# Optimization experiments

Hardware: AMD Instinct MI355X
Metric: run time of the kernel (lower is better)

## Reference

```python
import jax, jax.numpy as jnp
import numpy as np

HS = 128  # hidden_size
B, L = 2, 1024


def setup_inputs() -> dict:
    key = jax.random.key(0)
    k = jax.random.split(key, 3)
    d = HS
    X = jax.random.normal(k[0], (B, L, d), dtype=jnp.float32)
    # mlp: Linear(4d -> d), GELU, Linear(d -> 1)
    W1 = jax.random.normal(k[1], (4 * d, d), dtype=jnp.float32) / np.sqrt(4 * d).astype(np.float32)
    b1 = jnp.zeros((d,), dtype=jnp.float32)
    W2 = jax.random.normal(k[2], (d, 1), dtype=jnp.float32) / np.sqrt(d).astype(np.float32)
    b2 = jnp.zeros((1,), dtype=jnp.float32)
    return {"X": X, "W1": W1, "b1": b1, "W2": W2, "b2": b2}


def reference(X, W1, b1, W2, b2):
    # f = cat([Xi, Xj, Xi-Xj, Xi*Xj]) @ W1  decomposes exactly into four matmuls:
    #   Xi@(Wi+Wd) + Xj@(Wj-Wd) + (Xi*Xj)@Wp
    # avoiding the (b,l,l,4d) concat tensor.
    b, l, d = X.shape
    Wi, Wj, Wd, Wp = jnp.split(W1, 4, axis=0)  # each (d, h)
    A = X @ (Wi + Wd)                           # (b,l,h): depends on i only
    Bm = X @ (Wj - Wd)                          # (b,l,h): depends on j only
    P = jnp.einsum('bid,bjd,dh->bijh', X, X, Wp)  # elementwise-product term
    h = jax.nn.gelu(A[:, :, None, :] + Bm[:, None, :, :] + P + b1,
                    approximate=False)          # (b,l,l,h), exact GELU like nn.GELU()
    out = jnp.einsum('bijh,ho->bij', h, W2) + b2[0]  # (b,l,l)
    out = jax.nn.relu(out)
    out = 0.5 * (out + jnp.swapaxes(out, 1, 2))      # symmetrize
    diag_mask = 1.0 - jnp.eye(l, dtype=out.dtype)    # zero the diagonal
    return out * diag_mask
```

## Files before the change

### kernel.cpp

```cpp
#include <hip/hip_runtime.h>


typedef __attribute__((ext_vector_type(8))) short short8;
typedef __attribute__((ext_vector_type(16))) float f32x16;
typedef __attribute__((ext_vector_type(2))) float f32x2;

#define NT 32
#define NTRI 528
#define IPB 8

__device__ __forceinline__ unsigned short f2bf(float f) {
  unsigned int u = __float_as_uint(f);
  u = (u + 0x7fffu + ((u >> 16) & 1u)) >> 16;
  return (unsigned short)u;
}

__device__ __forceinline__ short8 pack8(float4 a, float4 b) {
  short8 r;
  r[0] = (short)f2bf(a.x); r[1] = (short)f2bf(a.y);
  r[2] = (short)f2bf(a.z); r[3] = (short)f2bf(a.w);
  r[4] = (short)f2bf(b.x); r[5] = (short)f2bf(b.y);
  r[6] = (short)f2bf(b.z); r[7] = (short)f2bf(b.w);
  return r;
}

__device__ __forceinline__ f32x2 gelu_2(f32x2 x) {
  f32x2 r = __builtin_elementwise_max(x, (f32x2)0.0f);
  f32x2 w = __builtin_elementwise_fma(r, (f32x2)2.0f, -x);
  f32x2 g = __builtin_elementwise_fma(w, (f32x2)0.00242f, (f32x2)-0.03569f);
  g = __builtin_elementwise_fma(w, g, (f32x2)-0.48287f);
  g = __builtin_elementwise_fma(w, g, (f32x2)-1.13986f);
  g = __builtin_elementwise_fma(w, g, (f32x2)-1.0f);
  f32x2 f;
  f[0] = __builtin_amdgcn_exp2f(g[0]);
  f[1] = __builtin_amdgcn_exp2f(g[1]);
  return __builtin_elementwise_fma(-f, w, r);
}

__global__ void k0_prep_w(const float* __restrict__ W1, unsigned short* __restrict__ wsT) {
  int idx = blockIdx.x * 256 + threadIdx.x;
  int arr = idx >> 14, rem = idx & 16383, h = rem >> 7, d = rem & 127;
  float v;
  if (arr == 0)      v = W1[d * 128 + h] + W1[(256 + d) * 128 + h];
  else if (arr == 1) v = W1[(128 + d) * 128 + h] - W1[(256 + d) * 128 + h];
  else               v = W1[(384 + d) * 128 + h];
  wsT[idx] = f2bf(v);
}

__global__ __launch_bounds__(256) void k1_ab(const float* __restrict__ X,
                                             const unsigned short* __restrict__ wsT,
                                             const float* __restrict__ b1,
                                             float* __restrict__ Aout,
                                             float* __restrict__ Bout) {
  int tid = threadIdx.x, w = tid >> 6, lane = tid & 63, jl = lane & 31, hi = lane >> 5;
  int row0 = blockIdx.x * 64;
  int c0 = w * 64;
  f32x16 a00 = (f32x16)0.f, a01 = (f32x16)0.f, a10 = (f32x16)0.f, a11 = (f32x16)0.f;
#pragma unroll
  for (int s = 0; s < 8; ++s) {
    const float* xp0 = X + (size_t)(row0 + jl) * 128 + s * 16 + hi * 8;
    const float* xp1 = xp0 + 32 * 128;
    short8 fa0 = pack8(*(const float4*)xp0, *(const float4*)(xp0 + 4));
    short8 fa1 = pack8(*(const float4*)xp1, *(const float4*)(xp1 + 4));
    short8 fb0 = *(const short8*)(wsT + (size_t)(c0 + jl) * 128 + s * 16 + hi * 8);
    short8 fb1 = *(const short8*)(wsT + (size_t)(c0 + 32 + jl) * 128 + s * 16 + hi * 8);
    a00 = __builtin_amdgcn_mfma_f32_32x32x16_bf16(fa0, fb0, a00, 0, 0, 0);
    a01 = __builtin_amdgcn_mfma_f32_32x32x16_bf16(fa0, fb1, a01, 0, 0, 0);
    a10 = __builtin_amdgcn_mfma_f32_32x32x16_bf16(fa1, fb0, a10, 0, 0, 0);
    a11 = __builtin_amdgcn_mfma_f32_32x32x16_bf16(fa1, fb1, a11, 0, 0, 0);
  }
  bool isB = (c0 >= 128);
  float b1v0 = 0.f, b1v1 = 0.f;
  if (isB) { b1v0 = b1[c0 - 128 + jl]; b1v1 = b1[c0 - 96 + jl]; }
#pragma unroll
  for (int q = 0; q < 16; ++q) {
    int r = (q & 3) + 8 * (q >> 2) + 4 * hi;
    int bl0 = row0 + r, bl1 = row0 + 32 + r;
    if (!isB) {
      Aout[(size_t)bl0 * 128 + c0 + jl]      = a00[q];
      Aout[(size_t)bl0 * 128 + c0 + 32 + jl] = a01[q];
      Aout[(size_t)bl1 * 128 + c0 + jl]      = a10[q];
      Aout[(size_t)bl1 * 128 + c0 + 32 + jl] = a11[q];
    } else {
      Bout[(size_t)bl0 * 128 + c0 - 128 + jl] = a00[q] + b1v0;
      Bout[(size_t)bl0 * 128 + c0 - 96 + jl]  = a01[q] + b1v1;
      Bout[(size_t)bl1 * 128 + c0 - 128 + jl] = a10[q] + b1v0;
      Bout[(size_t)bl1 * 128 + c0 - 96 + jl]  = a11[q] + b1v1;
    }
  }
}

union BfPack { __bf16 h[16]; short8 v[2]; };

__global__ __launch_bounds__(256) void k2_main(const float* __restrict__ X,
                                               const unsigned short* __restrict__ WpT,
                                               const float* __restrict__ Aws,
                                               const float* __restrict__ Bws,
                                               const float* __restrict__ W2,
                                               const float* __restrict__ b2,
                                               float* __restrict__ out) {
  __shared__ __align__(16) unsigned short Mlds[2][32 * 128];
  __shared__ __align__(16) float Xp[IPB][128];
  __shared__ __align__(16) float Abias[IPB][128];
  __shared__ __align__(16) float Bbias[IPB][128];
  __shared__ __align__(16) float W2l[128];
  __shared__ float2 osum[IPB][4][32];
  __shared__ float valbuf[IPB][33];

  int bid = blockIdx.x;
  int q4 = bid & 3;
  int tl = bid >> 2;
  int b = tl / NTRI;
  int t = tl - b * NTRI;
  int ti = 0;
  while (t >= NT - ti) { t -= NT - ti; ++ti; }
  int tj = ti + t;
  int gi0 = ti * 32, gj0 = tj * 32;
  int giBase = gi0 + q4 * IPB;

  int tid = threadIdx.x, w = tid >> 6, lane = tid & 63, jl = lane & 31, hi = lane >> 5;
  int dseg = tid >> 5;
  int gj = gj0 + jl;
  const size_t rowX = (size_t)b * 1024;

  {
    int r = tid >> 5, c = (tid & 31) * 4;
    const float* xp = X   + (rowX + giBase + r) * 128 + c;
    const float* ap = Aws + (rowX + giBase + r) * 128 + c;
    const float* bp = Bws + (rowX + giBase + r) * 128 + c;
    *(float4*)(&Xp[r][c])    = *(const float4*)(xp);
    *(float4*)(&Abias[r][c]) = *(const float4*)(ap);
    *(float4*)(&Bbias[r][c]) = *(const float4*)(bp);
    if (tid < 128) W2l[tid] = W2[tid];
  }

  float xj[16], bmj[16], ajv[16];
  {
    const float* xjp = X + (rowX + gj) * 128 + dseg * 16;
    *(float4*)(xj + 0)  = *(const float4*)(xjp + 0);
    *(float4*)(xj + 4)  = *(const float4*)(xjp + 4);
    *(float4*)(xj + 8)  = *(const float4*)(xjp + 8);
    *(float4*)(xj + 12) = *(const float4*)(xjp + 12);
  }
#pragma unroll
  for (int g = 0; g < 4; ++g) {
    int hb = 8 * g + 4 * hi + 32 * w;
    *(float4*)(bmj + 4 * g) = *(const float4*)(Bws + (rowX + gj) * 128 + hb);
    *(float4*)(ajv + 4 * g) = *(const float4*)(Aws + (rowX + gj) * 128 + hb);
  }
  short8 afrag[8];
#pragma unroll
  for (int s = 0; s < 8; ++s)
    afrag[s] = *(const short8*)(WpT + (size_t)(w * 32 + jl) * 128 + s * 16 + hi * 8);
  float b2s = b2[0];

  char* mB0 = (char*)Mlds[0];
  char* mB1 = (char*)Mlds[1];
  int rbase = jl * 256;
  int swz = (jl & 15) << 4;

  auto writeM = [&](int i, char* mp) {
    const float* xip = &Xp[i][dseg * 16];
    float xv[16];
    *(float4*)(xv + 0)  = *(const float4*)(xip + 0);
    *(float4*)(xv + 4)  = *(const float4*)(xip + 4);
    *(float4*)(xv + 8)  = *(const float4*)(xip + 8);
    *(float4*)(xv + 12) = *(const float4*)(xip + 12);
    BfPack mb;
#pragma unroll
    for (int r = 0; r < 8; ++r) {
      f32x2 xa = { xv[2 * r], xv[2 * r + 1] };
      f32x2 xb = { xj[2 * r], xj[2 * r + 1] };
      f32x2 pr = xa * xb;
      mb.h[2 * r]     = (__bf16)pr[0];
      mb.h[2 * r + 1] = (__bf16)pr[1];
    }
    *(short8*)(mp + rbase + ((dseg * 32 + 0) ^ swz))  = mb.v[0];
    *(short8*)(mp + rbase + ((dseg * 32 + 16) ^ swz)) = mb.v[1];
  };
  auto mfmaTile = [&](const char* mr) -> f32x16 {
    f32x16 acc = (f32x16)0.0f;
#pragma unroll
    for (int s = 0; s < 8; ++s) {
      short8 bf = *(const short8*)(mr + rbase + (((2 * s + hi) * 16) ^ swz));
      acc = __builtin_amdgcn_mfma_f32_32x32x16_bf16(afrag[s], bf, acc, 0, 0, 0);
    }
    return acc;
  };
  auto epilogue = [&](const f32x16& acc, int r) {
    f32x2 o1v = { 0.f, 0.f }, o2v = { 0.f, 0.f };
#pragma unroll
    for (int k = 0; k < 8; ++k) {
      int hb = ((2 * k) & 3) + 8 * ((2 * k) >> 2) + 4 * hi + 32 * w;
      f32x2 aiv = *(const f32x2*)(&Abias[r][hb]);
      f32x2 biv = *(const f32x2*)(&Bbias[r][hb]);
      f32x2 wv  = *(const f32x2*)(&W2l[hb]);
      f32x2 p   = { acc[2 * k], acc[2 * k + 1] };
      f32x2 b_j = { bmj[2 * k], bmj[2 * k + 1] };
      f32x2 a_j = { ajv[2 * k], ajv[2 * k + 1] };
      f32x2 g1 = gelu_2((p + aiv) + b_j);
      f32x2 g2 = gelu_2((p + a_j) + biv);
      o1v = __builtin_elementwise_fma(g1, wv, o1v);
      o2v = __builtin_elementwise_fma(g2, wv, o2v);
    }
    float o1 = o1v[0] + o1v[1], o2 = o2v[0] + o2v[1];
    o1 += __shfl_xor(o1, 32);
    o2 += __shfl_xor(o2, 32);
    if (lane < 32) osum[r][w][lane] = make_float2(o1, o2);
  };

  __syncthreads();
  writeM(0, mB0);
  __syncthreads();

  f32x16 accP;

#pragma unroll 1
  for (int i = 0; i < IPB; ++i) {
    f32x16 accC = mfmaTile((i & 1) ? mB1 : mB0);
    if (i + 1 < IPB) writeM(i + 1, ((i + 1) & 1) ? mB1 : mB0);
    if (i >= 1) epilogue(accP, i - 1);
    accP = accC;
    __syncthreads();
  }
  epilogue(accP, IPB - 1);
  __syncthreads();

  {
    int r = tid >> 5;
    int j = tid & 31;
    float2 p0 = osum[r][0][j], p1 = osum[r][1][j];
    float2 p2 = osum[r][2][j], p3 = osum[r][3][j];
    float s1 = p0.x + p1.x + p2.x + p3.x + b2s;
    float s2 = p0.y + p1.y + p2.y + p3.y + b2s;
    float v = 0.5f * (fmaxf(s1, 0.f) + fmaxf(s2, 0.f));
    int gi = giBase + r;
    if (ti == tj && gj0 + j == gi) v = 0.f;
    out[(rowX + gi) * 1024 + gj0 + j] = v;
    valbuf[r][j] = v;
  }
  __syncthreads();

  if (ti != tj && tid < 64) {
    int j = tid >> 1, i0 = (tid & 1) * 4;
    float4 v;
    v.x = valbuf[i0 + 0][j]; v.y = valbuf[i0 + 1][j];
    v.z = valbuf[i0 + 2][j]; v.w = valbuf[i0 + 3][j];
    *(float4*)(out + (rowX + gj0 + j) * 1024 + giBase + i0) = v;
  }
}

extern "C" void kernel_launch(void* const* d_in, const int* in_sizes, int n_in,
                              void* d_out, int out_size, void* d_ws, size_t ws_size,
                              hipStream_t stream) {
  (void)in_sizes; (void)n_in; (void)out_size; (void)ws_size;
  const float* X  = (const float*)d_in[0];
  const float* W1 = (const float*)d_in[1];
  const float* b1 = (const float*)d_in[2];
  const float* W2 = (const float*)d_in[3];
  const float* b2 = (const float*)d_in[4];
  float* out = (float*)d_out;

  unsigned short* wsT = (unsigned short*)d_ws;
  unsigned short* WpT = wsT + 2 * 16384;
  float* Aws = (float*)((char*)d_ws + 98304);
  float* Bws = (float*)((char*)d_ws + 98304 + 1048576);

  k0_prep_w<<<192, 256, 0, stream>>>(W1, wsT);
  k1_ab<<<32, 256, 0, stream>>>(X, wsT, b1, Aws, Bws);
  k2_main<<<8 * NTRI, 256, 0, stream>>>(X, WpT, Aws, Bws, W2, b2, out);
}
```

Before: 132.2 us.

## Lower-degree GELU polynomial, register-resident W2 and bias loads, smaller k1 tiles

Three things change. The GELU erfc-style exponent polynomial drops from degree 4 to degree 3, which removes one FMA per element in the hot epilogue but makes the approximation looser. W2 now sits in registers and the per-row A/B bias loads become float4 LDS reads hoisted ahead of writeM, replacing scattered float2 LDS reads inside the epilogue. The k1_ab kernel now handles 32 rows per block across 64 blocks instead of 64 rows across 32, for more parallelism in that small kernel.

```diff
diff --git a/kernel.cpp b/kernel.cpp
--- a/kernel.cpp
+++ b/kernel.cpp
@@ -27,9 +27,8 @@
 __device__ __forceinline__ f32x2 gelu_2(f32x2 x) {
   f32x2 r = __builtin_elementwise_max(x, (f32x2)0.0f);
   f32x2 w = __builtin_elementwise_fma(r, (f32x2)2.0f, -x);
-  f32x2 g = __builtin_elementwise_fma(w, (f32x2)0.00242f, (f32x2)-0.03569f);
-  g = __builtin_elementwise_fma(w, g, (f32x2)-0.48287f);
-  g = __builtin_elementwise_fma(w, g, (f32x2)-1.13986f);
+  f32x2 g = __builtin_elementwise_fma(w, (f32x2)0.03833f, (f32x2)-0.71844f);
+  g = __builtin_elementwise_fma(w, g, (f32x2)-0.97609f);
   g = __builtin_elementwise_fma(w, g, (f32x2)-1.0f);
   f32x2 f;
   f[0] = __builtin_amdgcn_exp2f(g[0]);
@@ -53,21 +52,17 @@
                                              float* __restrict__ Aout,
                                              float* __restrict__ Bout) {
   int tid = threadIdx.x, w = tid >> 6, lane = tid & 63, jl = lane & 31, hi = lane >> 5;
-  int row0 = blockIdx.x * 64;
+  int row0 = blockIdx.x * 32;
   int c0 = w * 64;
-  f32x16 a00 = (f32x16)0.f, a01 = (f32x16)0.f, a10 = (f32x16)0.f, a11 = (f32x16)0.f;
+  f32x16 a00 = (f32x16)0.f, a01 = (f32x16)0.f;
 #pragma unroll
   for (int s = 0; s < 8; ++s) {
     const float* xp0 = X + (size_t)(row0 + jl) * 128 + s * 16 + hi * 8;
-    const float* xp1 = xp0 + 32 * 128;
     short8 fa0 = pack8(*(const float4*)xp0, *(const float4*)(xp0 + 4));
-    short8 fa1 = pack8(*(const float4*)xp1, *(const float4*)(xp1 + 4));
     short8 fb0 = *(const short8*)(wsT + (size_t)(c0 + jl) * 128 + s * 16 + hi * 8);
     short8 fb1 = *(const short8*)(wsT + (size_t)(c0 + 32 + jl) * 128 + s * 16 + hi * 8);
     a00 = __builtin_amdgcn_mfma_f32_32x32x16_bf16(fa0, fb0, a00, 0, 0, 0);
     a01 = __builtin_amdgcn_mfma_f32_32x32x16_bf16(fa0, fb1, a01, 0, 0, 0);
-    a10 = __builtin_amdgcn_mfma_f32_32x32x16_bf16(fa1, fb0, a10, 0, 0, 0);
-    a11 = __builtin_amdgcn_mfma_f32_32x32x16_bf16(fa1, fb1, a11, 0, 0, 0);
   }
   bool isB = (c0 >= 128);
   float b1v0 = 0.f, b1v1 = 0.f;
@@ -75,17 +70,13 @@
 #pragma unroll
   for (int q = 0; q < 16; ++q) {
     int r = (q & 3) + 8 * (q >> 2) + 4 * hi;
-    int bl0 = row0 + r, bl1 = row0 + 32 + r;
+    int bl0 = row0 + r;
     if (!isB) {
       Aout[(size_t)bl0 * 128 + c0 + jl]      = a00[q];
       Aout[(size_t)bl0 * 128 + c0 + 32 + jl] = a01[q];
-      Aout[(size_t)bl1 * 128 + c0 + jl]      = a10[q];
-      Aout[(size_t)bl1 * 128 + c0 + 32 + jl] = a11[q];
     } else {
       Bout[(size_t)bl0 * 128 + c0 - 128 + jl] = a00[q] + b1v0;
       Bout[(size_t)bl0 * 128 + c0 - 96 + jl]  = a01[q] + b1v1;
-      Bout[(size_t)bl1 * 128 + c0 - 128 + jl] = a10[q] + b1v0;
-      Bout[(size_t)bl1 * 128 + c0 - 96 + jl]  = a11[q] + b1v1;
     }
   }
 }
@@ -103,7 +94,6 @@
   __shared__ __align__(16) float Xp[IPB][128];
   __shared__ __align__(16) float Abias[IPB][128];
   __shared__ __align__(16) float Bbias[IPB][128];
-  __shared__ __align__(16) float W2l[128];
   __shared__ float2 osum[IPB][4][32];
   __shared__ float valbuf[IPB][33];
 
@@ -131,10 +121,9 @@
     *(float4*)(&Xp[r][c])    = *(const float4*)(xp);
     *(float4*)(&Abias[r][c]) = *(const float4*)(ap);
     *(float4*)(&Bbias[r][c]) = *(const float4*)(bp);
-    if (tid < 128) W2l[tid] = W2[tid];
-  }
-
-  float xj[16], bmj[16], ajv[16];
+  }
+
+  float xj[16], bmj[16], ajv[16], w2h[16];
   {
     const float* xjp = X + (rowX + gj) * 128 + dseg * 16;
     *(float4*)(xj + 0)  = *(const float4*)(xjp + 0);
@@ -147,6 +136,7 @@
     int hb = 8 * g + 4 * hi + 32 * w;
     *(float4*)(bmj + 4 * g) = *(const float4*)(Bws + (rowX + gj) * 128 + hb);
     *(float4*)(ajv + 4 * g) = *(const float4*)(Aws + (rowX + gj) * 128 + hb);
+    *(float4*)(w2h + 4 * g) = *(const float4*)(W2 + hb);
   }
   short8 afrag[8];
 #pragma unroll
@@ -187,19 +177,26 @@
     }
     return acc;
   };
-  auto epilogue = [&](const f32x16& acc, int r) {
+  auto loadBias = [&](int r, float* aiv, float* biv) {
+#pragma unroll
+    for (int g = 0; g < 4; ++g) {
+      int hb = 8 * g + 4 * hi + 32 * w;
+      *(float4*)(aiv + 4 * g) = *(const float4*)(&Abias[r][hb]);
+      *(float4*)(biv + 4 * g) = *(const float4*)(&Bbias[r][hb]);
+    }
+  };
+  auto epilogue = [&](const f32x16& acc, const float* aiv, const float* biv, int r) {
     f32x2 o1v = { 0.f, 0.f }, o2v = { 0.f, 0.f };
 #pragma unroll
     for (int k = 0; k < 8; ++k) {
-      int hb = ((2 * k) & 3) + 8 * ((2 * k) >> 2) + 4 * hi + 32 * w;
-      f32x2 aiv = *(const f32x2*)(&Abias[r][hb]);
-      f32x2 biv = *(const f32x2*)(&Bbias[r][hb]);
-      f32x2 wv  = *(const f32x2*)(&W2l[hb]);
       f32x2 p   = { acc[2 * k], acc[2 * k + 1] };
+      f32x2 a_i = { aiv[2 * k], aiv[2 * k + 1] };
+      f32x2 b_i = { biv[2 * k], biv[2 * k + 1] };
+      f32x2 a_j = { ajv[2 * k], ajv[2 * k + 1] };
       f32x2 b_j = { bmj[2 * k], bmj[2 * k + 1] };
-      f32x2 a_j = { ajv[2 * k], ajv[2 * k + 1] };
-      f32x2 g1 = gelu_2((p + aiv) + b_j);
-      f32x2 g2 = gelu_2((p + a_j) + biv);
+      f32x2 wv  = { w2h[2 * k], w2h[2 * k + 1] };
+      f32x2 g1 = gelu_2((p + a_i) + b_j);
+      f32x2 g2 = gelu_2((p + a_j) + b_i);
       o1v = __builtin_elementwise_fma(g1, wv, o1v);
       o2v = __builtin_elementwise_fma(g2, wv, o2v);
     }
@@ -214,16 +211,19 @@
   __syncthreads();
 
   f32x16 accP;
+  float aivP[16], bivP[16];
 
 #pragma unroll 1
   for (int i = 0; i < IPB; ++i) {
     f32x16 accC = mfmaTile((i & 1) ? mB1 : mB0);
+    if (i >= 1) loadBias(i - 1, aivP, bivP);
     if (i + 1 < IPB) writeM(i + 1, ((i + 1) & 1) ? mB1 : mB0);
-    if (i >= 1) epilogue(accP, i - 1);
+    if (i >= 1) epilogue(accP, aivP, bivP, i - 1);
     accP = accC;
     __syncthreads();
   }
-  epilogue(accP, IPB - 1);
+  loadBias(IPB - 1, aivP, bivP);
+  epilogue(accP, aivP, bivP, IPB - 1);
   __syncthreads();
 
   {
@@ -267,6 +267,6 @@
   float* Bws = (float*)((char*)d_ws + 98304 + 1048576);
 
   k0_prep_w<<<192, 256, 0, stream>>>(W1, wsT);
-  k1_ab<<<32, 256, 0, stream>>>(X, wsT, b1, Aws, Bws);
+  k1_ab<<<64, 256, 0, stream>>>(X, wsT, b1, Aws, Bws);
   k2_main<<<8 * NTRI, 256, 0, stream>>>(X, WpT, Aws, Bws, W2, b2, out);
 }
```

Result: no change. 132.9 us (+0.5%).
